# Performance work log

Hardware: AMD Instinct MI355X
Metric: run time of the kernel (lower is better)

## Reference

```python
import jax, jax.numpy as jnp
import numpy as np

# Dims: batch=2, seqlen=L=384, d_inner=d=384, d_state=s=384, dt_rank=r=384, d_conv=4.
# NOTE: the original torch module only runs when L == d_inner == d_state == dt_rank
# (see its broadcasting in SelectiveScan and the Linear layer plumbing); we reproduce
# that exact (quirky) broadcast faithfully.
B_, L_, D_, S_, R_, K_ = 2, 384, 384, 384, 384, 4


def setup_inputs() -> dict:
    key = jax.random.key(0)
    ks = jax.random.split(key, 9)
    f32 = jnp.float32
    return {
        "x": jax.random.normal(ks[0], (B_, L_, D_), f32),
        "A_log": jax.random.normal(ks[1], (D_, S_), f32) * 0.02,
        "D": jax.random.normal(ks[2], (D_,), f32) * 0.02,
        "dt_w": jax.random.normal(ks[3], (D_, R_), f32) * 0.02,
        "dt_b": jax.random.normal(ks[4], (D_,), f32) * 0.02,
        "B_w": jax.random.normal(ks[5], (S_, D_), f32) * (1.0 / np.sqrt(D_)),
        "C_w": jax.random.normal(ks[6], (S_, D_), f32) * (1.0 / np.sqrt(D_)),
        "conv_w": jax.random.normal(ks[7], (D_, 1, K_), f32) * (1.0 / np.sqrt(K_)),
        "conv_b": jnp.zeros((D_,), f32),
    }


def _forward(x, A_log, D, dt_w, dt_b, B_w, C_w, conv_w, conv_b):
    b, L, d = x.shape
    A = -jnp.exp(A_log)                       # (d, s)
    dt = jax.nn.softplus(x @ dt_w.T + dt_b)   # (b, L, d)
    x_dbl = x @ B_w.T                         # (b, L, s)
    Bm = x_dbl @ B_w.T                        # (b, L, s)  (module applies B_proj twice)
    Cm = x_dbl @ C_w.T                        # (b, L, s)
    # causal depthwise conv1d: pad (k-1) on the left == torch pad k-1 then [:, :, :L]
    xc = jax.lax.conv_general_dilated(
        x.transpose(0, 2, 1), conv_w, (1,), [(conv_w.shape[-1] - 1, 0)],
        feature_group_count=d, dimension_numbers=("NCH", "OIH", "NCH"))
    xc = xc + conv_b[None, :, None]
    u = jax.nn.silu(xc.transpose(0, 2, 1))    # (b, L, d)
    # selective scan (faithful to the torch SelectiveScan broadcasting)
    deltaA = jnp.exp(dt[..., None] * A[None, None])          # (b, L, d, s)
    deltaB_u = dt[..., None] * Bm[:, None, :, :] * u[..., None]  # (b, L, d, s), needs L==d

    def step(h, inp):
        dA_i, dBu_i, C_i, u_i = inp
        h = dA_i * h + dBu_i                  # (b, d, s)
        y = jnp.sum(h * C_i[:, None, :], -1) + u_i * D  # (b, d)
        return h, y

    h0 = jnp.zeros((b, d, deltaA.shape[-1]), x.dtype)
    xs = (deltaA.transpose(1, 0, 2, 3), deltaB_u.transpose(1, 0, 2, 3),
          Cm.transpose(1, 0, 2), u.transpose(1, 0, 2))
    _, ys = jax.lax.scan(step, h0, xs)        # ys: (L, b, d)
    return ys.transpose(1, 0, 2)


def reference(x, A_log, D, dt_w, dt_b, B_w, C_w, conv_w, conv_b):
    return _forward(x, A_log, D, dt_w, dt_b, B_w, C_w, conv_w, conv_b)
```

## Files before the change

kernel.cpp:

```cpp
#include <hip/hip_runtime.h>
#include <math.h>

#define B_SZ 2
#define L_SZ 384
#define D_SZ 384
#define S_SZ 384
#define BLK_ELEMS (L_SZ * D_SZ)
#define TOT_ELEMS (B_SZ * L_SZ * D_SZ)
#define LOG2E 1.4426950408889634f

typedef __attribute__((ext_vector_type(8))) short bf16x8;
typedef __attribute__((ext_vector_type(4))) float f32x4;

__device__ __forceinline__ float fexp2(float x) {
  return __builtin_amdgcn_exp2f(x);
}
__device__ __forceinline__ float softplus_f(float z) {
  return (z > 20.f) ? z : log1pf(__expf(z));
}
__device__ __forceinline__ unsigned short f2bf(float f) {
  unsigned int u = __float_as_uint(f);
  return (unsigned short)((u + 0x7FFFu + ((u >> 16) & 1u)) >> 16);
}
#define PIPELINE_FENCE() asm volatile("" ::: "memory")

__global__ __launch_bounds__(256) void cvt_bf16_kernel(
    const float* __restrict__ x, const float* __restrict__ dt_w,
    const float* __restrict__ B_w, const float* __restrict__ C_w,
    unsigned short* __restrict__ xbf, unsigned short* __restrict__ dtwbf,
    unsigned short* __restrict__ Bwbf, unsigned short* __restrict__ Cwbf) {
  const int blk = blockIdx.x;
  const float* src;
  unsigned short* dst;
  int base;
  if (blk < 288) { src = x; dst = xbf; base = blk; }
  else if (blk < 432) { src = dt_w; dst = dtwbf; base = blk - 288; }
  else if (blk < 576) { src = B_w; dst = Bwbf; base = blk - 432; }
  else { src = C_w; dst = Cwbf; base = blk - 576; }
  const int idx = base * 1024 + threadIdx.x * 4;
  const float4 v = *(const float4*)(src + idx);
  ushort4 o;
  o.x = f2bf(v.x); o.y = f2bf(v.y); o.z = f2bf(v.z); o.w = f2bf(v.w);
  *(ushort4*)(dst + idx) = o;
}

template <int MODE>
__global__ __launch_bounds__(128, 2) void mfma_dual_gemm(
    const unsigned short* __restrict__ Abf,
    const unsigned short* __restrict__ W1bf,
    const unsigned short* __restrict__ W2bf,
    const float* __restrict__ bias,
    float* __restrict__ O1, void* __restrict__ O2v) {
  __shared__ unsigned short sA[32 * 392];
  __shared__ unsigned short sW1[16 * 392];
  __shared__ unsigned short sW2[16 * 392];

  const int t = threadIdx.x;
  const int wv = t >> 6;
  const int lane = t & 63;
  const int nt = blockIdx.x;
  const int mrow = blockIdx.y;

  const unsigned short* Ab = Abf + mrow * 32 * 384;
  const unsigned short* W1b = W1bf + nt * 16 * 384;
  const unsigned short* W2b = W2bf + nt * 16 * 384;

#pragma unroll
  for (int it = 0; it < 12; ++it) {
    const int id = t + it * 128;
    const int row = id / 48, col = id - row * 48;
    *(bf16x8*)&sA[row * 392 + col * 8] = *(const bf16x8*)(Ab + id * 8);
  }
#pragma unroll
  for (int it = 0; it < 6; ++it) {
    const int id = t + it * 128;
    const int row = id / 48, col = id - row * 48;
    *(bf16x8*)&sW1[row * 392 + col * 8] = *(const bf16x8*)(W1b + id * 8);
    *(bf16x8*)&sW2[row * 392 + col * 8] = *(const bf16x8*)(W2b + id * 8);
  }
  __syncthreads();

  const int rc = lane & 15;
  const int quad = lane >> 4;
  bf16x8 af[12], w1f[12], w2f[12];
#pragma unroll
  for (int kt = 0; kt < 12; ++kt) {
    af[kt] = *(const bf16x8*)&sA[(wv * 16 + rc) * 392 + quad * 8 + kt * 32];
    w1f[kt] = *(const bf16x8*)&sW1[rc * 392 + quad * 8 + kt * 32];
    w2f[kt] = *(const bf16x8*)&sW2[rc * 392 + quad * 8 + kt * 32];
  }
  PIPELINE_FENCE();
  f32x4 acc1 = {0.f, 0.f, 0.f, 0.f};
  f32x4 acc2 = {0.f, 0.f, 0.f, 0.f};
#pragma unroll
  for (int kt = 0; kt < 12; ++kt) {
    acc1 = __builtin_amdgcn_mfma_f32_16x16x32_bf16(af[kt], w1f[kt], acc1, 0, 0, 0);
    acc2 = __builtin_amdgcn_mfma_f32_16x16x32_bf16(af[kt], w2f[kt], acc2, 0, 0, 0);
  }
  const int col = nt * 16 + rc;
  const int row0 = mrow * 32 + wv * 16 + quad * 4;
  if constexpr (MODE == 1) {
    unsigned short* O2 = (unsigned short*)O2v;
    const float bb = bias[col];
#pragma unroll
    for (int r = 0; r < 4; ++r) {
      O1[(row0 + r) * 384 + col] = softplus_f(acc1[r] + bb);
      O2[(row0 + r) * 384 + col] = f2bf(acc2[r]);
    }
  } else {
    float* O2 = (float*)O2v;
#pragma unroll
    for (int r = 0; r < 4; ++r) {
      O1[(row0 + r) * 384 + col] = acc1[r];
      O2[(row0 + r) * 384 + col] = acc2[r];
    }
  }
}

__global__ __launch_bounds__(256) void conv_tr_kernel(
    const float* __restrict__ x, const float* __restrict__ cw,
    const float* __restrict__ cb, const float* __restrict__ dt,
    float* __restrict__ u, float* __restrict__ dt_t,
    float* __restrict__ dtu_t) {
  __shared__ float Tdt[32][33];
  __shared__ float Tdu[32][33];
  const int tx = threadIdx.x;
  const int ty = threadIdx.y;
  const int b = blockIdx.z;
  const int i0 = blockIdx.y * 32;
  const int l0 = blockIdx.x * 32;
  const int gi = i0 + tx;
  const float cbv = cb[gi];
  const float cw0 = cw[gi * 4 + 0], cw1 = cw[gi * 4 + 1];
  const float cw2 = cw[gi * 4 + 2], cw3 = cw[gi * 4 + 3];
#pragma unroll
  for (int r = 0; r < 4; ++r) {
    const int l = l0 + ty + 8 * r;
    float acc = cbv;
    const float x3 = x[(b * L_SZ + l) * D_SZ + gi];
    const float x2 = (l >= 1) ? x[(b * L_SZ + l - 1) * D_SZ + gi] : 0.f;
    const float x1 = (l >= 2) ? x[(b * L_SZ + l - 2) * D_SZ + gi] : 0.f;
    const float x0 = (l >= 3) ? x[(b * L_SZ + l - 3) * D_SZ + gi] : 0.f;
    acc = fmaf(x0, cw0, acc);
    acc = fmaf(x1, cw1, acc);
    acc = fmaf(x2, cw2, acc);
    acc = fmaf(x3, cw3, acc);
    const float uv = acc / (1.f + __expf(-acc));
    const int off = (b * L_SZ + l) * D_SZ + gi;
    u[off] = uv;
    const float dtv = dt[off];
    Tdt[ty + 8 * r][tx] = dtv;
    Tdu[ty + 8 * r][tx] = dtv * uv;
  }
  __syncthreads();
#pragma unroll
  for (int r = 0; r < 4; ++r) {
    const int il = ty + 8 * r;
    const int off = (b * D_SZ + i0 + il) * L_SZ + l0 + tx;
    dt_t[off] = Tdt[tx][il];
    dtu_t[off] = Tdu[tx][il];
  }
}

struct ChunkV {
  float combo;
  float c[16];
};

#define LOAD_CHUNK(K, B0, B1, B2, B3, B4, B5, CMB)                             \
  {                                                                            \
    asm volatile("global_load_dword %0, %1, off" : "=v"(K.combo) : "v"(CMB));  \
    asm volatile("global_load_dword %0, %1, off" : "=v"(K.c[0]) : "v"(B0));    \
    asm volatile("global_load_dword %0, %1, off offset:1536"                   \
                 : "=v"(K.c[1]) : "v"(B0));                                    \
    asm volatile("global_load_dword %0, %1, off offset:3072"                   \
                 : "=v"(K.c[2]) : "v"(B0));                                    \
    asm volatile("global_load_dword %0, %1, off" : "=v"(K.c[3]) : "v"(B1));    \
    asm volatile("global_load_dword %0, %1, off offset:1536"                   \
                 : "=v"(K.c[4]) : "v"(B1));                                    \
    asm volatile("global_load_dword %0, %1, off offset:3072"                   \
                 : "=v"(K.c[5]) : "v"(B1));                                    \
    asm volatile("global_load_dword %0, %1, off" : "=v"(K.c[6]) : "v"(B2));    \
    asm volatile("global_load_dword %0, %1, off offset:1536"                   \
                 : "=v"(K.c[7]) : "v"(B2));                                    \
    asm volatile("global_load_dword %0, %1, off offset:3072"                   \
                 : "=v"(K.c[8]) : "v"(B2));                                    \
    asm volatile("global_load_dword %0, %1, off" : "=v"(K.c[9]) : "v"(B3));    \
    asm volatile("global_load_dword %0, %1, off offset:1536"                   \
                 : "=v"(K.c[10]) : "v"(B3));                                   \
    asm volatile("global_load_dword %0, %1, off offset:3072"                   \
                 : "=v"(K.c[11]) : "v"(B3));                                   \
    asm volatile("global_load_dword %0, %1, off" : "=v"(K.c[12]) : "v"(B4));   \
    asm volatile("global_load_dword %0, %1, off offset:1536"                   \
                 : "=v"(K.c[13]) : "v"(B4));                                   \
    asm volatile("global_load_dword %0, %1, off offset:3072"                   \
                 : "=v"(K.c[14]) : "v"(B4));                                   \
    asm volatile("global_load_dword %0, %1, off" : "=v"(K.c[15]) : "v"(B5));   \
  }

#define WAIT_CHUNK(K)                                                          \
  asm volatile("s_waitcnt vmcnt(34)"                                           \
               : "+v"(K.combo), "+v"(K.c[0]), "+v"(K.c[1]), "+v"(K.c[2]),      \
                 "+v"(K.c[3]), "+v"(K.c[4]), "+v"(K.c[5]), "+v"(K.c[6]),       \
                 "+v"(K.c[7]), "+v"(K.c[8]), "+v"(K.c[9]), "+v"(K.c[10]),      \
                 "+v"(K.c[11]), "+v"(K.c[12]), "+v"(K.c[13]), "+v"(K.c[14]),   \
                 "+v"(K.c[15]))

#define ADV_BASES()                                                            \
  {                                                                            \
    cb0 += 6144; cb1 += 6144; cb2 += 6144;                                     \
    cb3 += 6144; cb4 += 6144; cb5 += 6144; cmb += 16;                          \
  }

__global__ __launch_bounds__(192, 3) void scan_kernel(
    const float* __restrict__ A_log, const float* __restrict__ dt_t,
    const float* __restrict__ dtu_t, const float* __restrict__ Bm,
    const float* __restrict__ Cm, float* __restrict__ part) {
  const int wave = blockIdx.x * 3 + (threadIdx.x >> 6);
  const int lane = threadIdx.x & 63;
  const int w = wave % 6;
  const int grp = wave / 6;
  const int b = grp / 192;
  const int i0 = (grp % 192) * 2;
  const int j = w * 64 + lane;

  const float al0 = A_log[(i0 + 0) * S_SZ + j];
  const float al1 = A_log[(i0 + 1) * S_SZ + j];
  const float bw0 = Bm[(b * D_SZ + i0 + 0) * S_SZ + j];
  const float bw1 = Bm[(b * D_SZ + i0 + 1) * S_SZ + j];
  const float a20 = -__expf(al0) * LOG2E;
  const float a21 = -__expf(al1) * LOG2E;
  float h0 = 0.f, h1 = 0.f;

  const int var = lane >> 5;
  const int cch = (lane >> 4) & 1;
  const int cs = lane & 15;
  const float* cmb =
      (var ? dtu_t : dt_t) + (b * D_SZ + i0 + cch) * L_SZ + cs;

  const float* cmrow = Cm + b * BLK_ELEMS + j;
  const float* cb0 = cmrow;
  const float* cb1 = cmrow + 3 * D_SZ;
  const float* cb2 = cmrow + 6 * D_SZ;
  const float* cb3 = cmrow + 9 * D_SZ;
  const float* cb4 = cmrow + 12 * D_SZ;
  const float* cb5 = cmrow + 15 * D_SZ;

  const int k = ((lane & 1) << 4) | ((lane & 2) << 2) | (lane & 4) |
                ((lane & 8) >> 2) | ((lane & 16) >> 4);
  float* pstore =
      part + ((w * B_SZ + b) * D_SZ + i0) * L_SZ + (k >> 4) * L_SZ + (k & 15);
  const bool storer = lane < 32;

  asm volatile("" :: "v"(a20), "v"(a21), "v"(bw0), "v"(bw1));
  asm volatile("s_waitcnt vmcnt(0)");

  auto compute_chunk = [&](ChunkV& K) {
    float acc[32];
    const int combo_i = __float_as_int(K.combo);
#pragma unroll
    for (int s = 0; s < 16; ++s) {
      const float dt0 = __int_as_float(__builtin_amdgcn_readlane(combo_i, s));
      const float dt1 =
          __int_as_float(__builtin_amdgcn_readlane(combo_i, 16 + s));
      const float du0 =
          __int_as_float(__builtin_amdgcn_readlane(combo_i, 32 + s));
      const float du1 =
          __int_as_float(__builtin_amdgcn_readlane(combo_i, 48 + s));
      const float e0 = fexp2(dt0 * a20);
      const float e1 = fexp2(dt1 * a21);
      h0 = fmaf(e0, h0, bw0 * du0);
      h1 = fmaf(e1, h1, bw1 * du1);
      acc[s] = h0 * K.c[s];
      acc[16 + s] = h1 * K.c[s];
    }
#pragma unroll
    for (int st = 0; st < 5; ++st) {
      const int d = 1 << st;
      const int n2 = 16 >> st;
      const bool hi = (lane & d) != 0;
#pragma unroll
      for (int q = 0; q < 16; ++q) {
        if (q < n2) {
          const float keep = hi ? acc[q + n2] : acc[q];
          const float send = hi ? acc[q] : acc[q + n2];
          acc[q] = keep + __shfl_xor(send, d, 64);
        }
      }
    }
    float r = acc[0];
    r += __shfl_xor(r, 32, 64);
    if (storer) *pstore = r;
    pstore += 16;
  };

  ChunkV K0, K1, K2;
  LOAD_CHUNK(K0, cb0, cb1, cb2, cb3, cb4, cb5, cmb);
  ADV_BASES();
  LOAD_CHUNK(K1, cb0, cb1, cb2, cb3, cb4, cb5, cmb);
  ADV_BASES();
#pragma unroll 1
  for (int mit = 0; mit < 8; ++mit) {
    LOAD_CHUNK(K2, cb0, cb1, cb2, cb3, cb4, cb5, cmb);
    ADV_BASES();
    WAIT_CHUNK(K0);
    compute_chunk(K0);
    LOAD_CHUNK(K0, cb0, cb1, cb2, cb3, cb4, cb5, cmb);
    ADV_BASES();
    WAIT_CHUNK(K1);
    compute_chunk(K1);
    LOAD_CHUNK(K1, cb0, cb1, cb2, cb3, cb4, cb5, cmb);
    ADV_BASES();
    WAIT_CHUNK(K2);
    compute_chunk(K2);
  }
}

__global__ __launch_bounds__(256) void combine_kernel(
    const float* __restrict__ part, const float* __restrict__ u,
    const float* __restrict__ Dv, float* __restrict__ y) {
  __shared__ float T[32][33];
  const int tx = threadIdx.x;
  const int ty0 = threadIdx.y;
  const int b = blockIdx.z;
  const int i0 = blockIdx.y * 32;
  const int l0 = blockIdx.x * 32;
#pragma unroll
  for (int r = 0; r < 4; ++r) {
    const int il = ty0 + 8 * r;
    float s = 0.f;
#pragma unroll
    for (int w = 0; w < 6; ++w)
      s += part[((w * B_SZ + b) * D_SZ + i0 + il) * L_SZ + l0 + tx];
    T[il][tx] = s;
  }
  __syncthreads();
#pragma unroll
  for (int r = 0; r < 4; ++r) {
    const int ll = ty0 + 8 * r;
    const int gi = i0 + tx;
    const int off = (b * L_SZ + l0 + ll) * D_SZ + gi;
    y[off] = fmaf(u[off], Dv[gi], T[tx][ll]);
  }
}

extern "C" void kernel_launch(void* const* d_in, const int* in_sizes, int n_in,
                              void* d_out, int out_size, void* d_ws,
                              size_t ws_size, hipStream_t stream) {
  const float* x = (const float*)d_in[0];
  const float* A_log = (const float*)d_in[1];
  const float* D = (const float*)d_in[2];
  const float* dt_w = (const float*)d_in[3];
  const float* dt_b = (const float*)d_in[4];
  const float* B_w = (const float*)d_in[5];
  const float* C_w = (const float*)d_in[6];
  const float* conv_w = (const float*)d_in[7];
  const float* conv_b = (const float*)d_in[8];
  float* y = (float*)d_out;

  float* ws = (float*)d_ws;
  float* dt = ws;
  float* u = ws + TOT_ELEMS;
  float* Bm = ws + 2 * TOT_ELEMS;
  float* Cm = ws + 3 * TOT_ELEMS;
  float* dt_t = ws + 4 * TOT_ELEMS;
  float* dtu_t = ws + 5 * TOT_ELEMS;
  float* part = ws + 6 * TOT_ELEMS;
  unsigned short* bfarea = (unsigned short*)(ws + 12 * TOT_ELEMS);
  unsigned short* xbf = bfarea;
  unsigned short* dtwbf = bfarea + 294912;
  unsigned short* Bwbf = bfarea + 442368;
  unsigned short* Cwbf = bfarea + 589824;
  unsigned short* xdblbf = bfarea + 737280;

  cvt_bf16_kernel<<<720, 256, 0, stream>>>(x, dt_w, B_w, C_w, xbf, dtwbf, Bwbf, Cwbf);
  mfma_dual_gemm<1><<<dim3(24, 24), 128, 0, stream>>>(xbf, dtwbf, Bwbf, dt_b, dt, xdblbf);
  mfma_dual_gemm<2><<<dim3(24, 24), 128, 0, stream>>>(xdblbf, Bwbf, Cwbf, nullptr, Bm, Cm);
  conv_tr_kernel<<<dim3(L_SZ / 32, D_SZ / 32, B_SZ), dim3(32, 8), 0, stream>>>(
      x, conv_w, conv_b, dt, u, dt_t, dtu_t);
  scan_kernel<<<768, 192, 0, stream>>>(A_log, dt_t, dtu_t, Bm, Cm, part);
  combine_kernel<<<dim3(L_SZ / 32, D_SZ / 32, B_SZ), dim3(32, 8), 0, stream>>>(
      part, u, D, y);
}
```

Before: 143.4 us.

## Restructure scan to one channel per wave with vector dt loads and DPP reductions

The scan kernel now gives each 64-lane wave a single d-channel instead of two, launching 4608 single-wave blocks rather than 768 three-wave blocks. Time chunks shrink from 16 to 8 steps, and dt/dt*u arrive through per-lane dwordx4 loads instead of readlane broadcasts. The butterfly reduction uses DPP row moves in place of several shuffles. This doubles the wave count and cuts register pressure and cross-lane cost, but C is loaded twice as often (once per channel rather than shared by two) and there are more loop iterations.

New measurement: 138.9 us. 1.03x faster.

```diff
diff --git a/kernel.cpp b/kernel.cpp
--- a/kernel.cpp
+++ b/kernel.cpp
@@ -23,6 +23,12 @@
   return (unsigned short)((u + 0x7FFFu + ((u >> 16) & 1u)) >> 16);
 }
 #define PIPELINE_FENCE() asm volatile("" ::: "memory")
+
+template <int CTRL>
+__device__ __forceinline__ float dpp_mov(float v) {
+  return __int_as_float(
+      __builtin_amdgcn_update_dpp(0, __float_as_int(v), CTRL, 0xF, 0xF, true));
+}
 
 __global__ __launch_bounds__(256) void cvt_bf16_kernel(
     const float* __restrict__ x, const float* __restrict__ dt_w,
@@ -162,14 +168,19 @@
   }
 }
 
-struct ChunkV {
-  float combo;
-  float c[16];
+struct ChunkS {
+  f32x4 d0, d1, u0, u1;
+  float c[8];
 };
 
-#define LOAD_CHUNK(K, B0, B1, B2, B3, B4, B5, CMB)                             \
+#define LOAD_CHUNK(K, B0, B1, B2, DTB, DUB)                                    \
   {                                                                            \
-    asm volatile("global_load_dword %0, %1, off" : "=v"(K.combo) : "v"(CMB));  \
+    asm volatile("global_load_dwordx4 %0, %1, off" : "=v"(K.d0) : "v"(DTB));   \
+    asm volatile("global_load_dwordx4 %0, %1, off offset:16"                   \
+                 : "=v"(K.d1) : "v"(DTB));                                     \
+    asm volatile("global_load_dwordx4 %0, %1, off" : "=v"(K.u0) : "v"(DUB));   \
+    asm volatile("global_load_dwordx4 %0, %1, off offset:16"                   \
+                 : "=v"(K.u1) : "v"(DUB));                                     \
     asm volatile("global_load_dword %0, %1, off" : "=v"(K.c[0]) : "v"(B0));    \
     asm volatile("global_load_dword %0, %1, off offset:1536"                   \
                  : "=v"(K.c[1]) : "v"(B0));                                    \
@@ -183,133 +194,107 @@
     asm volatile("global_load_dword %0, %1, off" : "=v"(K.c[6]) : "v"(B2));    \
     asm volatile("global_load_dword %0, %1, off offset:1536"                   \
                  : "=v"(K.c[7]) : "v"(B2));                                    \
-    asm volatile("global_load_dword %0, %1, off offset:3072"                   \
-                 : "=v"(K.c[8]) : "v"(B2));                                    \
-    asm volatile("global_load_dword %0, %1, off" : "=v"(K.c[9]) : "v"(B3));    \
-    asm volatile("global_load_dword %0, %1, off offset:1536"                   \
-                 : "=v"(K.c[10]) : "v"(B3));                                   \
-    asm volatile("global_load_dword %0, %1, off offset:3072"                   \
-                 : "=v"(K.c[11]) : "v"(B3));                                   \
-    asm volatile("global_load_dword %0, %1, off" : "=v"(K.c[12]) : "v"(B4));   \
-    asm volatile("global_load_dword %0, %1, off offset:1536"                   \
-                 : "=v"(K.c[13]) : "v"(B4));                                   \
-    asm volatile("global_load_dword %0, %1, off offset:3072"                   \
-                 : "=v"(K.c[14]) : "v"(B4));                                   \
-    asm volatile("global_load_dword %0, %1, off" : "=v"(K.c[15]) : "v"(B5));   \
   }
 
 #define WAIT_CHUNK(K)                                                          \
-  asm volatile("s_waitcnt vmcnt(34)"                                           \
-               : "+v"(K.combo), "+v"(K.c[0]), "+v"(K.c[1]), "+v"(K.c[2]),      \
-                 "+v"(K.c[3]), "+v"(K.c[4]), "+v"(K.c[5]), "+v"(K.c[6]),       \
-                 "+v"(K.c[7]), "+v"(K.c[8]), "+v"(K.c[9]), "+v"(K.c[10]),      \
-                 "+v"(K.c[11]), "+v"(K.c[12]), "+v"(K.c[13]), "+v"(K.c[14]),   \
-                 "+v"(K.c[15]))
+  asm volatile("s_waitcnt vmcnt(24)"                                           \
+               : "+v"(K.d0), "+v"(K.d1), "+v"(K.u0), "+v"(K.u1),               \
+                 "+v"(K.c[0]), "+v"(K.c[1]), "+v"(K.c[2]), "+v"(K.c[3]),       \
+                 "+v"(K.c[4]), "+v"(K.c[5]), "+v"(K.c[6]), "+v"(K.c[7]))
 
 #define ADV_BASES()                                                            \
-  {                                                                            \
-    cb0 += 6144; cb1 += 6144; cb2 += 6144;                                     \
-    cb3 += 6144; cb4 += 6144; cb5 += 6144; cmb += 16;                          \
-  }
-
-__global__ __launch_bounds__(192, 3) void scan_kernel(
+  { cb0 += 3072; cb1 += 3072; cb2 += 3072; dtB += 8; duB += 8; }
+
+__global__ __launch_bounds__(64, 4) void scan_kernel(
     const float* __restrict__ A_log, const float* __restrict__ dt_t,
     const float* __restrict__ dtu_t, const float* __restrict__ Bm,
     const float* __restrict__ Cm, float* __restrict__ part) {
-  const int wave = blockIdx.x * 3 + (threadIdx.x >> 6);
-  const int lane = threadIdx.x & 63;
+  const int wave = blockIdx.x;
+  const int lane = threadIdx.x;
   const int w = wave % 6;
-  const int grp = wave / 6;
-  const int b = grp / 192;
-  const int i0 = (grp % 192) * 2;
+  const int sid = wave / 6;
+  const int b = sid / D_SZ;
+  const int i = sid % D_SZ;
   const int j = w * 64 + lane;
 
-  const float al0 = A_log[(i0 + 0) * S_SZ + j];
-  const float al1 = A_log[(i0 + 1) * S_SZ + j];
-  const float bw0 = Bm[(b * D_SZ + i0 + 0) * S_SZ + j];
-  const float bw1 = Bm[(b * D_SZ + i0 + 1) * S_SZ + j];
-  const float a20 = -__expf(al0) * LOG2E;
-  const float a21 = -__expf(al1) * LOG2E;
-  float h0 = 0.f, h1 = 0.f;
-
-  const int var = lane >> 5;
-  const int cch = (lane >> 4) & 1;
-  const int cs = lane & 15;
-  const float* cmb =
-      (var ? dtu_t : dt_t) + (b * D_SZ + i0 + cch) * L_SZ + cs;
-
+  const float a2 = -__expf(A_log[i * S_SZ + j]) * LOG2E;
+  const float bw = Bm[(b * D_SZ + i) * S_SZ + j];
+  float h = 0.f;
+
+  const float* dtB = dt_t + (b * D_SZ + i) * L_SZ;
+  const float* duB = dtu_t + (b * D_SZ + i) * L_SZ;
   const float* cmrow = Cm + b * BLK_ELEMS + j;
   const float* cb0 = cmrow;
   const float* cb1 = cmrow + 3 * D_SZ;
   const float* cb2 = cmrow + 6 * D_SZ;
-  const float* cb3 = cmrow + 9 * D_SZ;
-  const float* cb4 = cmrow + 12 * D_SZ;
-  const float* cb5 = cmrow + 15 * D_SZ;
-
-  const int k = ((lane & 1) << 4) | ((lane & 2) << 2) | (lane & 4) |
-                ((lane & 8) >> 2) | ((lane & 16) >> 4);
-  float* pstore =
-      part + ((w * B_SZ + b) * D_SZ + i0) * L_SZ + (k >> 4) * L_SZ + (k & 15);
-  const bool storer = lane < 32;
-
-  asm volatile("" :: "v"(a20), "v"(a21), "v"(bw0), "v"(bw1));
+
+  const int sq = (((lane >> 3) & 1) << 2) | (((lane >> 2) & 1) << 1) | (lane & 1);
+  const bool storer = (lane & 0x32) == 0;
+  float* pstore = part + ((w * B_SZ + b) * D_SZ + i) * L_SZ + sq;
+
+  asm volatile("" :: "v"(a2), "v"(bw));
   asm volatile("s_waitcnt vmcnt(0)");
 
-  auto compute_chunk = [&](ChunkV& K) {
-    float acc[32];
-    const int combo_i = __float_as_int(K.combo);
-#pragma unroll
-    for (int s = 0; s < 16; ++s) {
-      const float dt0 = __int_as_float(__builtin_amdgcn_readlane(combo_i, s));
-      const float dt1 =
-          __int_as_float(__builtin_amdgcn_readlane(combo_i, 16 + s));
-      const float du0 =
-          __int_as_float(__builtin_amdgcn_readlane(combo_i, 32 + s));
-      const float du1 =
-          __int_as_float(__builtin_amdgcn_readlane(combo_i, 48 + s));
-      const float e0 = fexp2(dt0 * a20);
-      const float e1 = fexp2(dt1 * a21);
-      h0 = fmaf(e0, h0, bw0 * du0);
-      h1 = fmaf(e1, h1, bw1 * du1);
-      acc[s] = h0 * K.c[s];
-      acc[16 + s] = h1 * K.c[s];
-    }
-#pragma unroll
-    for (int st = 0; st < 5; ++st) {
-      const int d = 1 << st;
-      const int n2 = 16 >> st;
-      const bool hi = (lane & d) != 0;
-#pragma unroll
-      for (int q = 0; q < 16; ++q) {
-        if (q < n2) {
-          const float keep = hi ? acc[q + n2] : acc[q];
-          const float send = hi ? acc[q] : acc[q + n2];
-          acc[q] = keep + __shfl_xor(send, d, 64);
-        }
+  auto compute_chunk = [&](ChunkS& K) {
+    float acc[8];
+    const float dts[8] = {K.d0[0], K.d0[1], K.d0[2], K.d0[3],
+                          K.d1[0], K.d1[1], K.d1[2], K.d1[3]};
+    const float dus[8] = {K.u0[0], K.u0[1], K.u0[2], K.u0[3],
+                          K.u1[0], K.u1[1], K.u1[2], K.u1[3]};
+#pragma unroll
+    for (int s = 0; s < 8; ++s) {
+      const float e = fexp2(dts[s] * a2);
+      h = fmaf(e, h, bw * dus[s]);
+      acc[s] = h * K.c[s];
+    }
+    {
+      const bool hi = (lane & 8) != 0;
+#pragma unroll
+      for (int q = 0; q < 4; ++q) {
+        const float keep = hi ? acc[q + 4] : acc[q];
+        const float send = hi ? acc[q] : acc[q + 4];
+        acc[q] = keep + dpp_mov<0x140>(send);
       }
     }
+    {
+      const bool hi = (lane & 4) != 0;
+#pragma unroll
+      for (int q = 0; q < 2; ++q) {
+        const float keep = hi ? acc[q + 2] : acc[q];
+        const float send = hi ? acc[q] : acc[q + 2];
+        acc[q] = keep + dpp_mov<0x141>(send);
+      }
+    }
+    {
+      const bool hi = (lane & 1) != 0;
+      const float keep = hi ? acc[1] : acc[0];
+      const float send = hi ? acc[0] : acc[1];
+      acc[0] = keep + dpp_mov<0xB1>(send);
+    }
     float r = acc[0];
+    r += __shfl_xor(r, 2, 64);
+    r += __shfl_xor(r, 16, 64);
     r += __shfl_xor(r, 32, 64);
     if (storer) *pstore = r;
-    pstore += 16;
+    pstore += 8;
   };
 
-  ChunkV K0, K1, K2;
-  LOAD_CHUNK(K0, cb0, cb1, cb2, cb3, cb4, cb5, cmb);
+  ChunkS K0, K1, K2;
+  LOAD_CHUNK(K0, cb0, cb1, cb2, dtB, duB);
   ADV_BASES();
-  LOAD_CHUNK(K1, cb0, cb1, cb2, cb3, cb4, cb5, cmb);
+  LOAD_CHUNK(K1, cb0, cb1, cb2, dtB, duB);
   ADV_BASES();
 #pragma unroll 1
-  for (int mit = 0; mit < 8; ++mit) {
-    LOAD_CHUNK(K2, cb0, cb1, cb2, cb3, cb4, cb5, cmb);
+  for (int it = 0; it < 16; ++it) {
+    LOAD_CHUNK(K2, cb0, cb1, cb2, dtB, duB);
     ADV_BASES();
     WAIT_CHUNK(K0);
     compute_chunk(K0);
-    LOAD_CHUNK(K0, cb0, cb1, cb2, cb3, cb4, cb5, cmb);
+    LOAD_CHUNK(K0, cb0, cb1, cb2, dtB, duB);
     ADV_BASES();
     WAIT_CHUNK(K1);
     compute_chunk(K1);
-    LOAD_CHUNK(K1, cb0, cb1, cb2, cb3, cb4, cb5, cmb);
+    LOAD_CHUNK(K1, cb0, cb1, cb2, dtB, duB);
     ADV_BASES();
     WAIT_CHUNK(K2);
     compute_chunk(K2);
@@ -378,7 +363,7 @@
   mfma_dual_gemm<2><<<dim3(24, 24), 128, 0, stream>>>(xdblbf, Bwbf, Cwbf, nullptr, Bm, Cm);
   conv_tr_kernel<<<dim3(L_SZ / 32, D_SZ / 32, B_SZ), dim3(32, 8), 0, stream>>>(
       x, conv_w, conv_b, dt, u, dt_t, dtu_t);
-  scan_kernel<<<768, 192, 0, stream>>>(A_log, dt_t, dtu_t, Bm, Cm, part);
+  scan_kernel<<<6 * B_SZ * D_SZ, 64, 0, stream>>>(A_log, dt_t, dtu_t, Bm, Cm, part);
   combine_kernel<<<dim3(L_SZ / 32, D_SZ / 32, B_SZ), dim3(32, 8), 0, stream>>>(
       part, u, D, y);
 }
```
